# Kernel tuning notes

Measured on AMD Instinct MI355X. Metric: run time of the kernel, lower is better.

The kernel has to match this reference:

```python
import jax, jax.numpy as jnp
import numpy as np

B, N, D, NS, ITERS = 32, 2048, 512, 8, 3
EPS = 1e-8
SCALE = D ** -0.5
LN_EPS = 1e-5


def _ln(x, g, b):
    m = x.mean(-1, keepdims=True)
    v = ((x - m) ** 2).mean(-1, keepdims=True)
    return (x - m) * jax.lax.rsqrt(v + LN_EPS) * g + b


def setup_inputs() -> dict:
    key = jax.random.key(0)
    ks = iter(jax.random.split(key, 40))
    w = lambda *s: jax.random.normal(next(ks), s, jnp.float32) * 0.02
    inp = {
        'inputs': jax.random.normal(next(ks), (B, N, D), jnp.float32),
        'slot_noise': jax.random.normal(next(ks), (B, NS, D), jnp.float32),
        'slots_mu': jax.random.normal(next(ks), (1, 1, D), jnp.float32),
        'slots_logsigma': w(1, 1, D),
        'k_w': w(D, D), 'k_b': jnp.zeros((D,), jnp.float32),
        'v_w': w(D, D), 'v_b': jnp.zeros((D,), jnp.float32),
        'gru_w_ih': w(3 * D, D), 'gru_w_hh': w(3 * D, D),
        'gru_b_ih': jnp.zeros((3 * D,), jnp.float32),
        'gru_b_hh': jnp.zeros((3 * D,), jnp.float32),
        'ln_in_g': jnp.ones((D,), jnp.float32), 'ln_in_b': jnp.zeros((D,), jnp.float32),
        'ln_slots_g': jnp.ones((D,), jnp.float32), 'ln_slots_b': jnp.zeros((D,), jnp.float32),
        'ln_pre_g': jnp.ones((D,), jnp.float32), 'ln_pre_b': jnp.zeros((D,), jnp.float32),
        'mlp1_w': w(1024, D), 'mlp1_b': jnp.zeros((1024,), jnp.float32),
        'mlp2_w': w(1024, 1024), 'mlp2_b': jnp.zeros((1024,), jnp.float32),
        'mlp3_w': w(512, 1024), 'mlp3_b': jnp.zeros((512,), jnp.float32),
        'mlp4_w': w(256, 512), 'mlp4_b': jnp.zeros((256,), jnp.float32),
    }
    return inp


def reference(inputs, slot_noise, slots_mu, slots_logsigma, k_w, k_b, v_w, v_b,
              gru_w_ih, gru_w_hh, gru_b_ih, gru_b_hh,
              ln_in_g, ln_in_b, ln_slots_g, ln_slots_b, ln_pre_g, ln_pre_b,
              mlp1_w, mlp1_b, mlp2_w, mlp2_b, mlp3_w, mlp3_b, mlp4_w, mlp4_b):
    b, n, d = inputs.shape
    # stochastic slot init: mu + exp(logsigma) * noise  -> [b, ns, d]
    slots = slots_mu + jnp.exp(slots_logsigma) * slot_noise
    x = _ln(inputs, ln_in_g, ln_in_b)
    k = x @ k_w.T + k_b
    v = x @ v_w.T + v_b
    updates = slots
    for _ in range(ITERS):
        slots_prev = slots
        q = _ln(slots, ln_slots_g, ln_slots_b)
        dots = jnp.einsum('bid,bjd->bij', q, k) * SCALE  # [b, ns, n]
        attn = jax.nn.softmax(dots, axis=1) + EPS        # softmax over slot axis
        attn = attn / attn.sum(-1, keepdims=True)        # renorm over tokens
        updates = jnp.einsum('bjd,bij->bid', v, attn)    # [b, ns, d]
        # GRUCell(updates, slots_prev), then residual add of updates
        u = updates.reshape(-1, d)
        h = slots_prev.reshape(-1, d)
        gi = u @ gru_w_ih.T + gru_b_ih
        gh = h @ gru_w_hh.T + gru_b_hh
        i_r, i_z, i_n = jnp.split(gi, 3, axis=-1)
        h_r, h_z, h_n = jnp.split(gh, 3, axis=-1)
        r = jax.nn.sigmoid(i_r + h_r)
        z = jax.nn.sigmoid(i_z + h_z)
        nn_ = jnp.tanh(i_n + r * h_n)
        h_new = (1.0 - z) * nn_ + z * h
        slots = (u + h_new).reshape(b, -1, d)
    # output MLP with exact GELU (torch default)
    s = _ln(slots, ln_pre_g, ln_pre_b)
    s = jax.nn.gelu(s @ mlp1_w.T + mlp1_b, approximate=False)
    s = jax.nn.gelu(s @ mlp2_w.T + mlp2_b, approximate=False)
    s = jax.nn.gelu(s @ mlp3_w.T + mlp3_b, approximate=False)
    s = s @ mlp4_w.T + mlp4_b
    return (updates, s)
```

## Files before the change

### kernel.cpp

```cpp
#include <hip/hip_runtime.h>
#include <math.h>

#define Bb 32
#define Nn 2048
#define Dd 512
#define NS 8
#define ITERS 3
#define EPSf 1e-8f
#define SCALEf 0.04419417382415922f
#define LN_EPSf 1e-5f

#define QHS 520
#define PTS 136
#define CHUNKS 16

typedef _Float16 half8 __attribute__((ext_vector_type(8)));
typedef float f32x4 __attribute__((ext_vector_type(4)));

__device__ __forceinline__ float waveReduceSum(float v) {
    #pragma unroll
    for (int m = 32; m >= 1; m >>= 1) v += __shfl_xor(v, m);
    return v;
}

__device__ __forceinline__ float gelu_exact(float x) {
    return 0.5f * x * (1.0f + erff(x * 0.7071067811865476f));
}

__device__ __forceinline__ void async_copy16(const _Float16* g, _Float16* l) {
    __builtin_amdgcn_global_load_lds(
        (const __attribute__((address_space(1))) unsigned int*)g,
        (__attribute__((address_space(3))) unsigned int*)l, 16, 0, 0);
}

__global__ __launch_bounds__(256) void megapack_kernel(
    const float* __restrict__ k_w, const float* __restrict__ v_w,
    const float* __restrict__ w_ih, const float* __restrict__ w_hh,
    const float* __restrict__ m1, const float* __restrict__ m2,
    const float* __restrict__ m3, const float* __restrict__ m4,
    _Float16* __restrict__ Bkv, _Float16* __restrict__ Bih, _Float16* __restrict__ Bhh,
    _Float16* __restrict__ Bm1, _Float16* __restrict__ Bm2,
    _Float16* __restrict__ Bm3, _Float16* __restrict__ Bm4) {
    int bid = blockIdx.x, tid = threadIdx.x;
    const float* src; _Float16* dst; int kbits, base;
    if (bid < 2048) {
        int i = bid * 256 + tid;
        Bkv[i] = (_Float16)(i < 262144 ? k_w[i] : v_w[i - 262144]);
        return;
    }
    else if (bid < 5120)  { src = w_ih; dst = Bih; kbits = 9;  base = 2048; }
    else if (bid < 8192)  { src = w_hh; dst = Bhh; kbits = 9;  base = 5120; }
    else if (bid < 10240) { src = m1;   dst = Bm1; kbits = 9;  base = 8192; }
    else if (bid < 14336) { src = m2;   dst = Bm2; kbits = 10; base = 10240; }
    else if (bid < 16384) { src = m3;   dst = Bm3; kbits = 10; base = 14336; }
    else                  { src = m4;   dst = Bm4; kbits = 9;  base = 16384; }
    int e = (bid - base) * 256 + tid;
    int K = 1 << kbits;
    int row = e >> kbits, k = e & (K - 1);
    _Float16 h = (_Float16)src[e];
    _Float16* d = dst + ((size_t)row << (kbits + 1));
    d[k] = h;
    d[K + k] = h;
}

__global__ __launch_bounds__(256) void pack_ln_single_kernel(
    const float* __restrict__ x, const float* __restrict__ g, const float* __restrict__ b,
    _Float16* __restrict__ Ap) {
    int wid = blockIdx.x * 4 + (threadIdx.x >> 6);
    int lane = threadIdx.x & 63;
    const float4* row4 = (const float4*)(x + (size_t)wid * Dd);
    float4 va = row4[lane * 2], vb = row4[lane * 2 + 1];
    float v[8] = {va.x, va.y, va.z, va.w, vb.x, vb.y, vb.z, vb.w};
    float s = 0.f, sq = 0.f;
    #pragma unroll
    for (int t = 0; t < 8; ++t) { s += v[t]; sq += v[t] * v[t]; }
    s = waveReduceSum(s);
    sq = waveReduceSum(sq);
    float m = s * (1.0f / Dd);
    float var = sq * (1.0f / Dd) - m * m;
    float rs = rsqrtf(var + LN_EPSf);
    const float4* g4 = (const float4*)g;
    const float4* b4 = (const float4*)b;
    float4 ga = g4[lane * 2], gb = g4[lane * 2 + 1];
    float4 ba = b4[lane * 2], bb = b4[lane * 2 + 1];
    float gg[8] = {ga.x, ga.y, ga.z, ga.w, gb.x, gb.y, gb.z, gb.w};
    float bbv[8] = {ba.x, ba.y, ba.z, ba.w, bb.x, bb.y, bb.z, bb.w};
    half8 o;
    #pragma unroll
    for (int t = 0; t < 8; ++t) o[t] = (_Float16)((v[t] - m) * rs * gg[t] + bbv[t]);
    *(half8*)(Ap + (size_t)wid * Dd + lane * 8) = o;
}

__global__ __launch_bounds__(256) void slots_init_kernel(
    const float* __restrict__ noise, const float* __restrict__ mu,
    const float* __restrict__ ls, float* __restrict__ slots, _Float16* __restrict__ A2,
    const float* __restrict__ lns_g, const float* __restrict__ lns_b,
    _Float16* __restrict__ qh) {
    int row = blockIdx.x * 4 + (threadIdx.x >> 6);
    int lane = threadIdx.x & 63;
    float val[8];
    float s = 0.f, sq = 0.f;
    #pragma unroll
    for (int t = 0; t < 8; ++t) {
        int d = t * 64 + lane;
        float v = mu[d] + expf(ls[d]) * noise[(size_t)row * 512 + d];
        val[t] = v;
        s += v; sq += v * v;
        slots[(size_t)row * 512 + d] = v;
        _Float16 hi = (_Float16)v;
        A2[(size_t)(256 + row) * 1024 + d] = hi;
        A2[(size_t)(256 + row) * 1024 + 512 + d] = (_Float16)(v - (float)hi);
    }
    s = waveReduceSum(s);
    sq = waveReduceSum(sq);
    float m = s * (1.0f / Dd);
    float var = sq * (1.0f / Dd) - m * m;
    float rs = rsqrtf(var + LN_EPSf);
    #pragma unroll
    for (int t = 0; t < 8; ++t) {
        int d = t * 64 + lane;
        qh[(size_t)row * 512 + d] = (_Float16)(((val[t] - m) * rs * lns_g[d] + lns_b[d]) * SCALEf);
    }
}

__global__ __launch_bounds__(256) void kv_hgemm_kernel(
    const _Float16* __restrict__ Apack, const _Float16* __restrict__ Bkv,
    const float* __restrict__ k_b, const float* __restrict__ v_b,
    _Float16* __restrict__ khalf, _Float16* __restrict__ vT) {
    __shared__ _Float16 smem[17408];
    _Float16* As = smem;
    _Float16* Bs = smem + 8192;
    const int f = blockIdx.x;
    const int m0 = ((f & 7) + ((f >> 6) << 3)) * 128;
    const int n0 = ((f >> 3) & 7) * 128;
    const int tid = threadIdx.x;
    const int w = tid >> 6, lane = tid & 63;
    const int r8 = lane >> 3, seg = lane & 7;
    const int lr = lane & 15, quad = lane >> 4;
    const int wm = w >> 1, wn = w & 1;
    f32x4 acc[4][4];
    #pragma unroll
    for (int i = 0; i < 4; ++i)
        #pragma unroll
        for (int j = 0; j < 4; ++j) acc[i][j] = (f32x4){0.f, 0.f, 0.f, 0.f};
    for (int k0 = 0; k0 < 512; k0 += 64) {
        __syncthreads();
        #pragma unroll
        for (int g = 0; g < 4; ++g) {
            int grp = w * 4 + g;
            int row = grp * 8 + r8;
            async_copy16(Apack + (size_t)(m0 + row) * 512 + k0 + seg * 8, As + grp * 512);
            async_copy16(Bkv + (size_t)(n0 + row) * 512 + k0 + seg * 8, Bs + grp * 512);
        }
        __syncthreads();
        #pragma unroll
        for (int kk = 0; kk < 2; ++kk) {
            half8 a[4], b[4];
            #pragma unroll
            for (int t = 0; t < 4; ++t) {
                a[t] = *(const half8*)(As + (wm * 64 + t * 16 + lr) * 64 + kk * 32 + quad * 8);
                b[t] = *(const half8*)(Bs + (wn * 64 + t * 16 + lr) * 64 + kk * 32 + quad * 8);
            }
            #pragma unroll
            for (int mt = 0; mt < 4; ++mt)
                #pragma unroll
                for (int nt = 0; nt < 4; ++nt)
                    acc[mt][nt] = __builtin_amdgcn_mfma_f32_16x16x32_f16(
                        a[mt], b[nt], acc[mt][nt], 0, 0, 0);
        }
    }
    __syncthreads();
    const bool isK = (n0 < 512);
    #pragma unroll
    for (int mt = 0; mt < 4; ++mt)
        #pragma unroll
        for (int nt = 0; nt < 4; ++nt) {
            int ml = wm * 64 + mt * 16 + quad * 4;
            int nl = wn * 64 + nt * 16 + lr;
            float bv = isK ? k_b[n0 + nl] : v_b[n0 - 512 + nl];
            #pragma unroll
            for (int r = 0; r < 4; ++r) {
                _Float16 h = (_Float16)(acc[mt][nt][r] + bv);
                if (isK) smem[(ml + r) * 136 + nl] = h;
                else     smem[nl * 136 + ml + r] = h;
            }
        }
    __syncthreads();
    int r = tid >> 1, half = tid & 1;
    _Float16* dst;
    if (isK) {
        dst = khalf + (size_t)(m0 + r) * 512 + n0 + half * 64;
    } else {
        int b = m0 >> 11, j0 = m0 & 2047, d0 = n0 - 512;
        dst = vT + ((size_t)b * 512 + d0 + r) * 2048 + j0 + half * 64;
    }
    #pragma unroll
    for (int c = 0; c < 8; ++c)
        *(half8*)(dst + c * 8) = *(const half8*)(smem + r * 136 + half * 64 + c * 8);
}

__global__ __launch_bounds__(256) void attn_kernel(
    const _Float16* __restrict__ qh_g,
    const _Float16* __restrict__ khalf, const _Float16* __restrict__ vT,
    float* __restrict__ rawp, float* __restrict__ sumsp) {
    const int b = blockIdx.y, chunk = blockIdx.x;
    __shared__ _Float16 qh[16 * QHS];
    __shared__ _Float16 pT[16 * PTS];
    __shared__ float sums_lds[64];
    const int tid = threadIdx.x, w = tid >> 6, lane = tid & 63;
    const int lr = lane & 15, quad = lane >> 4;

    {
        int r = tid >> 5;
        int c = (tid & 31) * 16;
        *(half8*)(qh + r * QHS + c) = *(const half8*)(qh_g + ((size_t)b * NS + r) * 512 + c);
        *(half8*)(qh + r * QHS + c + 8) = *(const half8*)(qh_g + ((size_t)b * NS + r) * 512 + c + 8);
        half8 z = {};
        *(half8*)(qh + (8 + r) * QHS + c) = z;
        *(half8*)(qh + (8 + r) * QHS + c + 8) = z;
    }
    __syncthreads();

    const int j0 = chunk * 128 + w * 32;
    f32x4 dots[2];
    dots[0] = (f32x4){0.f, 0.f, 0.f, 0.f};
    dots[1] = (f32x4){0.f, 0.f, 0.f, 0.f};
    for (int ks = 0; ks < 16; ++ks) {
        half8 bq = *(const half8*)(qh + lr * QHS + ks * 32 + quad * 8);
        #pragma unroll
        for (int mf = 0; mf < 2; ++mf) {
            half8 ak = *(const half8*)(khalf + ((size_t)b * Nn + j0 + mf * 16 + lr) * 512 + ks * 32 + quad * 8);
            dots[mf] = __builtin_amdgcn_mfma_f32_16x16x32_f16(ak, bq, dots[mf], 0, 0, 0);
        }
    }
    float ssum = 0.f;
    #pragma unroll
    for (int mf = 0; mf < 2; ++mf) {
        f32x4 d = dots[mf];
        f32x4 mx = d;
        #pragma unroll
        for (int msk = 1; msk <= 4; msk <<= 1) {
            #pragma unroll
            for (int r = 0; r < 4; ++r) mx[r] = fmaxf(mx[r], __shfl_xor(mx[r], msk));
        }
        f32x4 p;
        #pragma unroll
        for (int r = 0; r < 4; ++r) p[r] = __expf(d[r] - mx[r]);
        f32x4 sm = p;
        #pragma unroll
        for (int msk = 1; msk <= 4; msk <<= 1) {
            #pragma unroll
            for (int r = 0; r < 4; ++r) sm[r] += __shfl_xor(sm[r], msk);
        }
        #pragma unroll
        for (int r = 0; r < 4; ++r) {
            _Float16 ph = (_Float16)(p[r] / sm[r] + EPSf);
            pT[lr * PTS + w * 32 + mf * 16 + quad * 4 + r] = ph;
            ssum += (float)ph;
        }
    }
    ssum += __shfl_xor(ssum, 16);
    ssum += __shfl_xor(ssum, 32);
    if (lane < 16) sums_lds[w * 16 + lane] = ssum;
    __syncthreads();

    f32x4 acc[8];
    #pragma unroll
    for (int nf = 0; nf < 8; ++nf) acc[nf] = (f32x4){0.f, 0.f, 0.f, 0.f};
    #pragma unroll
    for (int kc = 0; kc < 4; ++kc) {
        half8 ap = *(const half8*)(pT + lr * PTS + kc * 32 + quad * 8);
        #pragma unroll
        for (int nf = 0; nf < 8; ++nf) {
            int dcol = w * 128 + nf * 16 + lr;
            half8 bv = *(const half8*)(vT + ((size_t)b * 512 + dcol) * 2048 + chunk * 128 + kc * 32 + quad * 8);
            acc[nf] = __builtin_amdgcn_mfma_f32_16x16x32_f16(ap, bv, acc[nf], 0, 0, 0);
        }
    }
    if (quad < 2) {
        #pragma unroll
        for (int nf = 0; nf < 8; ++nf) {
            #pragma unroll
            for (int r = 0; r < 4; ++r) {
                int slot = quad * 4 + r;
                rawp[(((size_t)chunk * Bb + b) * NS + slot) * Dd + w * 128 + nf * 16 + lr] = acc[nf][r];
            }
        }
    }
    if (w == 0 && lane < NS) {
        float tot = sums_lds[lane] + sums_lds[16 + lane] + sums_lds[32 + lane] + sums_lds[48 + lane];
        sumsp[((size_t)chunk * Bb + b) * NS + lane] = tot;
    }
}

__global__ __launch_bounds__(256) void finalize_kernel(
    const float* __restrict__ rawp, const float* __restrict__ sumsp,
    float* __restrict__ u, float* __restrict__ out0, _Float16* __restrict__ A2) {
    int idx = blockIdx.x * 256 + threadIdx.x;
    int row = idx >> 9, k = idx & 511;
    float rs = 0.f, ss = 0.f;
    #pragma unroll
    for (int c = 0; c < CHUNKS; ++c) {
        rs += rawp[(size_t)c * 131072 + idx];
        ss += sumsp[c * 256 + row];
    }
    float val = rs / ss;
    u[idx] = val;
    out0[idx] = val;
    _Float16 hi = (_Float16)val;
    A2[(size_t)row * 1024 + k] = hi;
    A2[(size_t)row * 1024 + 512 + k] = (_Float16)(val - (float)hi);
}

__device__ __forceinline__ void hgemm64_core(
    const _Float16* __restrict__ A, const _Float16* __restrict__ Bw,
    int K2, f32x4 acc[2][2], _Float16* As, _Float16* Bs) {
    const int tid = threadIdx.x;
    const int w = tid >> 6, lane = tid & 63;
    const int r8 = lane >> 3, seg = lane & 7;
    const int lr = lane & 15, quad = lane >> 4;
    const int wm = w >> 1, wn = w & 1;
    for (int k0 = 0; k0 < K2; k0 += 64) {
        __syncthreads();
        #pragma unroll
        for (int p = 0; p < 2; ++p) {
            int grp = p * 4 + w;
            int row = grp * 8 + r8;
            async_copy16(A + (size_t)row * K2 + k0 + seg * 8, As + grp * 512);
            async_copy16(Bw + (size_t)row * K2 + k0 + seg * 8, Bs + grp * 512);
        }
        __syncthreads();
        #pragma unroll
        for (int kk = 0; kk < 2; ++kk) {
            half8 a[2], b[2];
            #pragma unroll
            for (int t = 0; t < 2; ++t) {
                a[t] = *(const half8*)(As + (wm * 32 + t * 16 + lr) * 64 + kk * 32 + quad * 8);
                b[t] = *(const half8*)(Bs + (wn * 32 + t * 16 + lr) * 64 + kk * 32 + quad * 8);
            }
            #pragma unroll
            for (int mt = 0; mt < 2; ++mt)
                #pragma unroll
                for (int nt = 0; nt < 2; ++nt)
                    acc[mt][nt] = __builtin_amdgcn_mfma_f32_16x16x32_f16(
                        a[mt], b[nt], acc[mt][nt], 0, 0, 0);
        }
    }
}

template <int ACT, int PACK>
__global__ __launch_bounds__(256) void hgemm64_kernel(
    const _Float16* __restrict__ A, const _Float16* __restrict__ Bw,
    const float* __restrict__ bias, float* __restrict__ C, _Float16* __restrict__ P,
    int K2, int N, int Kp) {
    __shared__ _Float16 As[4096], Bs[4096];
    const int m0 = blockIdx.y * 64, n0 = blockIdx.x * 64;
    f32x4 acc[2][2];
    #pragma unroll
    for (int i = 0; i < 2; ++i)
        #pragma unroll
        for (int j = 0; j < 2; ++j) acc[i][j] = (f32x4){0.f, 0.f, 0.f, 0.f};
    hgemm64_core(A + (size_t)m0 * K2, Bw + (size_t)n0 * K2, K2, acc, As, Bs);
    const int tid = threadIdx.x;
    const int w = tid >> 6, lane = tid & 63;
    const int lr = lane & 15, quad = lane >> 4;
    const int wm = w >> 1, wn = w & 1;
    #pragma unroll
    for (int mt = 0; mt < 2; ++mt)
        #pragma unroll
        for (int nt = 0; nt < 2; ++nt) {
            int n = n0 + wn * 32 + nt * 16 + lr;
            float bv = bias[n];
            #pragma unroll
            for (int r = 0; r < 4; ++r) {
                int m = m0 + wm * 32 + mt * 16 + quad * 4 + r;
                float val = acc[mt][nt][r] + bv;
                if (ACT) val = gelu_exact(val);
                if (PACK) {
                    _Float16 hi = (_Float16)val;
                    P[(size_t)m * 2 * Kp + n] = hi;
                    P[(size_t)m * 2 * Kp + Kp + n] = (_Float16)(val - (float)hi);
                } else {
                    C[(size_t)m * N + n] = val;
                }
            }
        }
}

__global__ __launch_bounds__(256) void gru_gemm_kernel(
    const _Float16* __restrict__ A2, const _Float16* __restrict__ Bih,
    const _Float16* __restrict__ Bhh, const float* __restrict__ b_ih,
    const float* __restrict__ b_hh, float* __restrict__ gi, float* __restrict__ gh) {
    __shared__ _Float16 As[4096], Bs[4096];
    const int by = blockIdx.y;
    const int n0 = blockIdx.x * 64;
    const _Float16* Ap; const _Float16* Bw; const float* bias; float* C;
    if (by < 4) { Ap = A2 + (size_t)by * 64 * 1024;        Bw = Bih; bias = b_ih; C = gi + (size_t)by * 64 * 1536; }
    else        { Ap = A2 + (size_t)(256 + (by - 4) * 64) * 1024; Bw = Bhh; bias = b_hh; C = gh + (size_t)(by - 4) * 64 * 1536; }
    f32x4 acc[2][2];
    #pragma unroll
    for (int i = 0; i < 2; ++i)
        #pragma unroll
        for (int j = 0; j < 2; ++j) acc[i][j] = (f32x4){0.f, 0.f, 0.f, 0.f};
    hgemm64_core(Ap, Bw + (size_t)n0 * 1024, 1024, acc, As, Bs);
    const int tid = threadIdx.x;
    const int w = tid >> 6, lane = tid & 63;
    const int lr = lane & 15, quad = lane >> 4;
    const int wm = w >> 1, wn = w & 1;
    #pragma unroll
    for (int mt = 0; mt < 2; ++mt)
        #pragma unroll
        for (int nt = 0; nt < 2; ++nt) {
            int n = n0 + wn * 32 + nt * 16 + lr;
            float bv = bias[n];
            #pragma unroll
            for (int r = 0; r < 4; ++r) {
                int m = wm * 32 + mt * 16 + quad * 4 + r;
                C[(size_t)m * 1536 + n] = acc[mt][nt][r] + bv;
            }
        }
}

__global__ __launch_bounds__(256) void gru_elem_kernel(
    const float* __restrict__ gi, const float* __restrict__ gh,
    const float* __restrict__ u, float* __restrict__ slots, _Float16* __restrict__ A2,
    const float* __restrict__ lns_g, const float* __restrict__ lns_b,
    _Float16* __restrict__ qh,
    const float* __restrict__ lnp_g, const float* __restrict__ lnp_b,
    _Float16* __restrict__ P1, int last) {
    int row = blockIdx.x * 4 + (threadIdx.x >> 6);
    int lane = threadIdx.x & 63;
    const float* gir = gi + (size_t)row * 1536;
    const float* ghr = gh + (size_t)row * 1536;
    float val[8];
    #pragma unroll
    for (int t = 0; t < 8; ++t) {
        int d = t * 64 + lane;
        float ir = gir[d], iz = gir[512 + d], in_ = gir[1024 + d];
        float hr = ghr[d], hz = ghr[512 + d], hn = ghr[1024 + d];
        float r = 1.0f / (1.0f + expf(-(ir + hr)));
        float z = 1.0f / (1.0f + expf(-(iz + hz)));
        float n = tanhf(in_ + r * hn);
        float h = slots[(size_t)row * 512 + d];
        float hnew = (1.0f - z) * n + z * h;
        float vv = u[(size_t)row * 512 + d] + hnew;
        val[t] = vv;
        slots[(size_t)row * 512 + d] = vv;
        _Float16 hi = (_Float16)vv;
        A2[(size_t)(256 + row) * 1024 + d] = hi;
        A2[(size_t)(256 + row) * 1024 + 512 + d] = (_Float16)(vv - (float)hi);
    }
    float s = 0.f, sq = 0.f;
    #pragma unroll
    for (int t = 0; t < 8; ++t) { s += val[t]; sq += val[t] * val[t]; }
    s = waveReduceSum(s);
    sq = waveReduceSum(sq);
    float m = s * (1.0f / Dd);
    float var = sq * (1.0f / Dd) - m * m;
    float rs = rsqrtf(var + LN_EPSf);
    if (!last) {
        #pragma unroll
        for (int t = 0; t < 8; ++t) {
            int d = t * 64 + lane;
            qh[(size_t)row * 512 + d] =
                (_Float16)(((val[t] - m) * rs * lns_g[d] + lns_b[d]) * SCALEf);
        }
    } else {
        #pragma unroll
        for (int t = 0; t < 8; ++t) {
            int d = t * 64 + lane;
            float a = (val[t] - m) * rs * lnp_g[d] + lnp_b[d];
            _Float16 hi = (_Float16)a;
            P1[(size_t)row * 1024 + d] = hi;
            P1[(size_t)row * 1024 + 512 + d] = (_Float16)(a - (float)hi);
        }
    }
}

extern "C" void kernel_launch(void* const* d_in, const int* in_sizes, int n_in,
                              void* d_out, int out_size, void* d_ws, size_t ws_size,
                              hipStream_t stream) {
    const float* inputs   = (const float*)d_in[0];
    const float* noise    = (const float*)d_in[1];
    const float* mu       = (const float*)d_in[2];
    const float* lsig     = (const float*)d_in[3];
    const float* k_w      = (const float*)d_in[4];
    const float* k_b      = (const float*)d_in[5];
    const float* v_w      = (const float*)d_in[6];
    const float* v_b      = (const float*)d_in[7];
    const float* w_ih     = (const float*)d_in[8];
    const float* w_hh     = (const float*)d_in[9];
    const float* b_ih     = (const float*)d_in[10];
    const float* b_hh     = (const float*)d_in[11];
    const float* ln_in_g  = (const float*)d_in[12];
    const float* ln_in_b  = (const float*)d_in[13];
    const float* ln_s_g   = (const float*)d_in[14];
    const float* ln_s_b   = (const float*)d_in[15];
    const float* ln_p_g   = (const float*)d_in[16];
    const float* ln_p_b   = (const float*)d_in[17];
    const float* mlp1_w   = (const float*)d_in[18];
    const float* mlp1_b   = (const float*)d_in[19];
    const float* mlp2_w   = (const float*)d_in[20];
    const float* mlp2_b   = (const float*)d_in[21];
    const float* mlp3_w   = (const float*)d_in[22];
    const float* mlp3_b   = (const float*)d_in[23];
    const float* mlp4_w   = (const float*)d_in[24];
    const float* mlp4_b   = (const float*)d_in[25];
    float* out0 = (float*)d_out;
    float* out1 = (float*)d_out + Bb * NS * Dd;

    char* wp = (char*)d_ws;
    auto alloc = [&](size_t bytes) -> void* {
        void* p = (void*)wp;
        wp += (bytes + 255) & ~(size_t)255;
        return p;
    };
    const size_t MR = (size_t)Bb * Nn;
    _Float16* Apack = (_Float16*)alloc(MR * 512 * 2);
    _Float16* khalf = (_Float16*)alloc(MR * 512 * 2);
    _Float16* vT    = (_Float16*)alloc((size_t)Bb * 512 * Nn * 2);
    _Float16* Bkv   = (_Float16*)alloc((size_t)1024 * 512 * 2);
    _Float16* Bih   = (_Float16*)alloc((size_t)1536 * 1024 * 2);
    _Float16* Bhh   = (_Float16*)alloc((size_t)1536 * 1024 * 2);
    _Float16* Bm1   = (_Float16*)alloc((size_t)1024 * 1024 * 2);
    _Float16* Bm2   = (_Float16*)alloc((size_t)1024 * 2048 * 2);
    _Float16* Bm3   = (_Float16*)alloc((size_t)512 * 2048 * 2);
    _Float16* Bm4   = (_Float16*)alloc((size_t)256 * 1024 * 2);
    float* slots    = (float*)alloc((size_t)Bb * NS * Dd * 4);
    _Float16* qh    = (_Float16*)alloc((size_t)Bb * NS * Dd * 2);
    float* rawp     = (float*)alloc((size_t)CHUNKS * Bb * NS * Dd * 4);
    float* sumsp    = (float*)alloc((size_t)CHUNKS * Bb * NS * 4);
    float* ubuf     = (float*)alloc((size_t)Bb * NS * Dd * 4);
    float* gi       = (float*)alloc((size_t)Bb * NS * 1536 * 4);
    float* gh       = (float*)alloc((size_t)Bb * NS * 1536 * 4);
    _Float16* A2    = (_Float16*)alloc((size_t)512 * 1024 * 2);
    _Float16* P1    = (_Float16*)alloc((size_t)256 * 1024 * 2);
    _Float16* P2    = (_Float16*)alloc((size_t)256 * 2048 * 2);
    _Float16* P3    = (_Float16*)alloc((size_t)256 * 2048 * 2);
    _Float16* P4    = (_Float16*)alloc((size_t)256 * 1024 * 2);

    megapack_kernel<<<16896, 256, 0, stream>>>(
        k_w, v_w, w_ih, w_hh, mlp1_w, mlp2_w, mlp3_w, mlp4_w,
        Bkv, Bih, Bhh, Bm1, Bm2, Bm3, Bm4);
    pack_ln_single_kernel<<<MR / 4, 256, 0, stream>>>(inputs, ln_in_g, ln_in_b, Apack);
    slots_init_kernel<<<64, 256, 0, stream>>>(noise, mu, lsig, slots, A2, ln_s_g, ln_s_b, qh);

    kv_hgemm_kernel<<<4096, 256, 0, stream>>>(Apack, Bkv, k_b, v_b, khalf, vT);

    for (int it = 0; it < ITERS; ++it) {
        attn_kernel<<<dim3(CHUNKS, Bb), 256, 0, stream>>>(qh, khalf, vT, rawp, sumsp);
        finalize_kernel<<<512, 256, 0, stream>>>(rawp, sumsp, ubuf, out0, A2);
        gru_gemm_kernel<<<dim3(24, 8), 256, 0, stream>>>(A2, Bih, Bhh, b_ih, b_hh, gi, gh);
        gru_elem_kernel<<<64, 256, 0, stream>>>(gi, gh, ubuf, slots, A2,
                                                ln_s_g, ln_s_b, qh,
                                                ln_p_g, ln_p_b, P1, it == ITERS - 1 ? 1 : 0);
    }

    hgemm64_kernel<1, 1><<<dim3(16, 4), 256, 0, stream>>>(P1, Bm1, mlp1_b, nullptr, P2, 1024, 1024, 1024);
    hgemm64_kernel<1, 1><<<dim3(16, 4), 256, 0, stream>>>(P2, Bm2, mlp2_b, nullptr, P3, 2048, 1024, 1024);
    hgemm64_kernel<1, 1><<<dim3(8, 4), 256, 0, stream>>>(P3, Bm3, mlp3_b, nullptr, P4, 2048, 512, 512);
    hgemm64_kernel<0, 0><<<dim3(4, 4), 256, 0, stream>>>(P4, Bm4, mlp4_b, out1, nullptr, 1024, 256, 256);
}
```

Baseline: 656.8 us.

## Rewrite K/V projection GEMM as 256x256 tiles with double-buffered swizzled LDS pipeline

Replaces the 128x128-tile K/V GEMM with a 256x256-tile, 512-thread kernel that double-buffers A/B tiles in LDS with XOR swizzling and interleaves async global-to-LDS copies with MFMA phases using explicit waitcnt, barriers and priority hints. The block index is remapped for locality and the epilogue writes through a swizzled LDS staging buffer. The aim is to hide global load latency, cut LDS bank conflicts and raise arithmetic intensity per block, at the cost of 128 KB LDS per block, higher register pressure and fragile hand-tuned wait counts.

New measurement: 599.8 us. -8.7%, faster.

```diff
diff --git a/kernel.cpp b/kernel.cpp
--- a/kernel.cpp
+++ b/kernel.cpp
@@ -123,80 +123,136 @@
     }
 }
 
-__global__ __launch_bounds__(256) void kv_hgemm_kernel(
+
+#define KV_PHASE(MQ, NQ, STG1, STG2, WAITOP)                                          \
+  {                                                                                   \
+    half8 af[4][2], bf[2][2];                                                         \
+    _Pragma("unroll") for (int mt = 0; mt < 4; ++mt)                                  \
+      _Pragma("unroll") for (int kk = 0; kk < 2; ++kk) {                              \
+        int R = wm * 128 + MQ * 64 + mt * 16 + lr;                                    \
+        af[mt][kk] = *(const half8*)(Alds + R * 64 +                                  \
+                     ((((kk << 2) | quad) ^ (lr & 7)) << 3));                         \
+      }                                                                               \
+    _Pragma("unroll") for (int nt = 0; nt < 2; ++nt)                                  \
+      _Pragma("unroll") for (int kk = 0; kk < 2; ++kk) {                              \
+        int R = wn * 64 + NQ * 32 + nt * 16 + lr;                                     \
+        bf[nt][kk] = *(const half8*)(Blds + R * 64 +                                  \
+                     ((((kk << 2) | quad) ^ (lr & 7)) << 3));                         \
+      }                                                                               \
+    STG1; STG2;                                                                       \
+    __builtin_amdgcn_s_barrier();                                                     \
+    asm volatile("s_waitcnt lgkmcnt(0)" ::: "memory");                                \
+    __builtin_amdgcn_sched_barrier(0);                                                \
+    __builtin_amdgcn_s_setprio(1);                                                    \
+    _Pragma("unroll") for (int mt = 0; mt < 4; ++mt)                                  \
+      _Pragma("unroll") for (int nt = 0; nt < 2; ++nt)                                \
+        _Pragma("unroll") for (int kk = 0; kk < 2; ++kk)                              \
+          acc[MQ * 4 + mt][NQ * 2 + nt] = __builtin_amdgcn_mfma_f32_16x16x32_f16(     \
+              af[mt][kk], bf[nt][kk], acc[MQ * 4 + mt][NQ * 2 + nt], 0, 0, 0);        \
+    __builtin_amdgcn_s_setprio(0);                                                    \
+    WAITOP;                                                                           \
+    __builtin_amdgcn_s_barrier();                                                     \
+  }
+
+__global__ __launch_bounds__(512, 2) void kv_hgemm256_kernel(
     const _Float16* __restrict__ Apack, const _Float16* __restrict__ Bkv,
     const float* __restrict__ k_b, const float* __restrict__ v_b,
     _Float16* __restrict__ khalf, _Float16* __restrict__ vT) {
-    __shared__ _Float16 smem[17408];
-    _Float16* As = smem;
-    _Float16* Bs = smem + 8192;
+    __shared__ _Float16 lds[4][16384];
     const int f = blockIdx.x;
-    const int m0 = ((f & 7) + ((f >> 6) << 3)) * 128;
-    const int n0 = ((f >> 3) & 7) * 128;
+    const int swz = ((f & 7) << 7) + (f >> 3);
+    const int m0 = (swz >> 2) << 8;
+    const int n0 = (swz & 3) << 8;
     const int tid = threadIdx.x;
-    const int w = tid >> 6, lane = tid & 63;
-    const int r8 = lane >> 3, seg = lane & 7;
+    const int lane = tid & 63;
+    const int wid = tid >> 6;
     const int lr = lane & 15, quad = lane >> 4;
-    const int wm = w >> 1, wn = w & 1;
-    f32x4 acc[4][4];
-    #pragma unroll
-    for (int i = 0; i < 4; ++i)
+    const int wm = wid >> 2, wn = wid & 3;
+    const int grow = tid >> 3;
+    const int sslot = ((tid & 7) ^ (grow & 7)) << 3;
+    const int lwave = wid << 9;
+
+    f32x4 acc[8][4];
+    #pragma unroll
+    for (int i = 0; i < 8; ++i)
         #pragma unroll
         for (int j = 0; j < 4; ++j) acc[i][j] = (f32x4){0.f, 0.f, 0.f, 0.f};
-    for (int k0 = 0; k0 < 512; k0 += 64) {
-        __syncthreads();
-        #pragma unroll
-        for (int g = 0; g < 4; ++g) {
-            int grp = w * 4 + g;
-            int row = grp * 8 + r8;
-            async_copy16(Apack + (size_t)(m0 + row) * 512 + k0 + seg * 8, As + grp * 512);
-            async_copy16(Bkv + (size_t)(n0 + row) * 512 + k0 + seg * 8, Bs + grp * 512);
-        }
-        __syncthreads();
-        #pragma unroll
-        for (int kk = 0; kk < 2; ++kk) {
-            half8 a[4], b[4];
-            #pragma unroll
-            for (int t = 0; t < 4; ++t) {
-                a[t] = *(const half8*)(As + (wm * 64 + t * 16 + lr) * 64 + kk * 32 + quad * 8);
-                b[t] = *(const half8*)(Bs + (wn * 64 + t * 16 + lr) * 64 + kk * 32 + quad * 8);
+
+    auto stageA = [&](int ktile, int par, int g) {
+        const _Float16* src = Apack + (size_t)(m0 + (g << 6) + grow) * 512 +
+                              ((ktile & 7) << 6) + sslot;
+        async_copy16(src, &lds[par * 2][(g << 12) + lwave]);
+    };
+    auto stageB = [&](int ktile, int par, int g) {
+        const _Float16* src = Bkv + (size_t)(n0 + (g << 6) + grow) * 512 +
+                              ((ktile & 7) << 6) + sslot;
+        async_copy16(src, &lds[par * 2 + 1][(g << 12) + lwave]);
+    };
+
+    stageA(0, 0, 0); stageA(0, 0, 2);
+    stageB(0, 0, 0); stageB(0, 0, 1); stageB(0, 0, 2); stageB(0, 0, 3);
+    stageA(0, 0, 1); stageA(1, 1, 0);
+    stageA(0, 0, 3); stageA(1, 1, 2);
+    asm volatile("s_waitcnt vmcnt(4)" ::: "memory");
+    __builtin_amdgcn_s_barrier();
+
+    #pragma unroll 2
+    for (int t = 0; t < 8; ++t) {
+        const int cur = t & 1, nxt = cur ^ 1;
+        const _Float16* Alds = &lds[cur * 2][0];
+        const _Float16* Blds = &lds[cur * 2 + 1][0];
+        KV_PHASE(0, 0, stageB(t + 1, nxt, 0), stageB(t + 1, nxt, 1), );
+        KV_PHASE(0, 1, stageB(t + 1, nxt, 2), stageB(t + 1, nxt, 3),
+                 asm volatile("s_waitcnt vmcnt(5)" ::: "memory"));
+        KV_PHASE(1, 0, stageA(t + 1, nxt, 1), stageA(t + 2, cur, 0), );
+        KV_PHASE(1, 1, stageA(t + 1, nxt, 3), stageA(t + 2, cur, 2),
+                 asm volatile("s_waitcnt vmcnt(4)" ::: "memory"));
+    }
+
+    asm volatile("s_waitcnt vmcnt(0)" ::: "memory");
+    __builtin_amdgcn_s_barrier();
+
+    _Float16* Cs = &lds[0][0];
+    const bool isK = (n0 < 512);
+    #pragma unroll
+    for (int mt = 0; mt < 8; ++mt)
+        #pragma unroll
+        for (int nt = 0; nt < 4; ++nt) {
+            int n = wn * 64 + nt * 16 + lr;
+            float bv = isK ? k_b[n0 + n] : v_b[n0 - 512 + n];
+            #pragma unroll
+            for (int r = 0; r < 4; ++r) {
+                int m = wm * 128 + mt * 16 + quad * 4 + r;
+                float val = acc[mt][nt][r] + bv;
+                int row = isK ? m : n;
+                int col = isK ? n : m;
+                int byt = (row << 9) + ((col << 1) ^ ((row & 7) << 4));
+                *(_Float16*)((char*)Cs + byt) = (_Float16)val;
             }
-            #pragma unroll
-            for (int mt = 0; mt < 4; ++mt)
-                #pragma unroll
-                for (int nt = 0; nt < 4; ++nt)
-                    acc[mt][nt] = __builtin_amdgcn_mfma_f32_16x16x32_f16(
-                        a[mt], b[nt], acc[mt][nt], 0, 0, 0);
-        }
-    }
-    __syncthreads();
-    const bool isK = (n0 < 512);
-    #pragma unroll
-    for (int mt = 0; mt < 4; ++mt)
-        #pragma unroll
-        for (int nt = 0; nt < 4; ++nt) {
-            int ml = wm * 64 + mt * 16 + quad * 4;
-            int nl = wn * 64 + nt * 16 + lr;
-            float bv = isK ? k_b[n0 + nl] : v_b[n0 - 512 + nl];
-            #pragma unroll
-            for (int r = 0; r < 4; ++r) {
-                _Float16 h = (_Float16)(acc[mt][nt][r] + bv);
-                if (isK) smem[(ml + r) * 136 + nl] = h;
-                else     smem[nl * 136 + ml + r] = h;
-            }
-        }
-    __syncthreads();
-    int r = tid >> 1, half = tid & 1;
-    _Float16* dst;
+        }
+    asm volatile("s_waitcnt lgkmcnt(0)" ::: "memory");
+    __builtin_amdgcn_s_barrier();
+
+    const int rr = (wid << 1) + (lane >> 5);
+    const int sl = lane & 31;
     if (isK) {
-        dst = khalf + (size_t)(m0 + r) * 512 + n0 + half * 64;
+        _Float16* dst0 = khalf + (size_t)m0 * 512 + n0;
+        #pragma unroll
+        for (int p = 0; p < 16; ++p) {
+            int row = p * 16 + rr;
+            int byt = (row << 9) + (((sl ^ (row & 7)) & 31) << 4);
+            *(half8*)(dst0 + (size_t)row * 512 + sl * 8) = *(const half8*)((char*)Cs + byt);
+        }
     } else {
         int b = m0 >> 11, j0 = m0 & 2047, d0 = n0 - 512;
-        dst = vT + ((size_t)b * 512 + d0 + r) * 2048 + j0 + half * 64;
-    }
-    #pragma unroll
-    for (int c = 0; c < 8; ++c)
-        *(half8*)(dst + c * 8) = *(const half8*)(smem + r * 136 + half * 64 + c * 8);
+        _Float16* dst0 = vT + ((size_t)b * 512 + d0) * 2048 + j0;
+        #pragma unroll
+        for (int p = 0; p < 16; ++p) {
+            int row = p * 16 + rr;
+            int byt = (row << 9) + (((sl ^ (row & 7)) & 31) << 4);
+            *(half8*)(dst0 + (size_t)row * 2048 + sl * 8) = *(const half8*)((char*)Cs + byt);
+        }
+    }
 }
 
 __global__ __launch_bounds__(256) void attn_kernel(
@@ -545,7 +601,7 @@
     pack_ln_single_kernel<<<MR / 4, 256, 0, stream>>>(inputs, ln_in_g, ln_in_b, Apack);
     slots_init_kernel<<<64, 256, 0, stream>>>(noise, mu, lsig, slots, A2, ln_s_g, ln_s_b, qh);
 
-    kv_hgemm_kernel<<<4096, 256, 0, stream>>>(Apack, Bkv, k_b, v_b, khalf, vT);
+    kv_hgemm256_kernel<<<1024, 512, 0, stream>>>(Apack, Bkv, k_b, v_b, khalf, vT);
 
     for (int it = 0; it < ITERS; ++it) {
         attn_kernel<<<dim3(CHUNKS, Bb), 256, 0, stream>>>(qh, khalf, vT, rawp, sumsp);
```
